# Optimization experiments

Measured on AMD Instinct MI355X. Metric: run time of the kernel, lower is better.

Reference implementation:

```python
import jax, jax.numpy as jnp
import numpy as np

EMBED_DIM = 2048
NUM_HEADS = 16
HEAD_DIM = EMBED_DIM // NUM_HEADS
B, T = 4, 2048


def setup_inputs() -> dict:
    key = jax.random.key(0)
    ks = jax.random.split(key, 9)
    s = 1.0 / np.sqrt(EMBED_DIM)
    x = jax.random.normal(ks[0], (B, T, EMBED_DIM), dtype=jnp.float32)
    Wq = jax.random.normal(ks[1], (EMBED_DIM, EMBED_DIM), dtype=jnp.float32) * s
    bq = jnp.zeros((EMBED_DIM,), dtype=jnp.float32)
    Wk = jax.random.normal(ks[2], (EMBED_DIM, EMBED_DIM), dtype=jnp.float32) * s
    bk = jnp.zeros((EMBED_DIM,), dtype=jnp.float32)
    Wv = jax.random.normal(ks[3], (EMBED_DIM, EMBED_DIM), dtype=jnp.float32) * s
    bv = jnp.zeros((EMBED_DIM,), dtype=jnp.float32)
    Wo = jax.random.normal(ks[4], (EMBED_DIM, EMBED_DIM), dtype=jnp.float32) * s
    bo = jnp.zeros((EMBED_DIM,), dtype=jnp.float32)
    return {"x": x, "Wq": Wq, "bq": bq, "Wk": Wk, "bk": bk,
            "Wv": Wv, "bv": bv, "Wo": Wo, "bo": bo}


def reference(x, Wq, bq, Wk, bk, Wv, bv, Wo, bo):
    Bb, Tt, C = x.shape
    H, D = NUM_HEADS, C // NUM_HEADS
    # QKV projections (Linear: x @ W.T + b), reshape to [B, H, T, D]
    q = (jnp.einsum('btc,oc->bto', x, Wq) + bq).reshape(Bb, Tt, H, D).transpose(0, 2, 1, 3)
    k = (jnp.einsum('btc,oc->bto', x, Wk) + bk).reshape(Bb, Tt, H, D).transpose(0, 2, 1, 3)
    v = (jnp.einsum('btc,oc->bto', x, Wv) + bv).reshape(Bb, Tt, H, D).transpose(0, 2, 1, 3)
    logits = jnp.einsum('bhqd,bhkd->bhqk', q, k) / jnp.sqrt(jnp.float32(D))
    causal = jnp.triu(jnp.ones((Tt, Tt), dtype=bool), 1)  # True above diagonal
    logits = jnp.where(causal, -jnp.inf, logits)
    attn = jax.nn.softmax(logits, axis=-1)
    out = jnp.einsum('bhqk,bhkd->bhqd', attn, v)  # [B, H, T, D]
    out = out.transpose(0, 2, 1, 3).reshape(Bb, Tt, C)
    y = jnp.einsum('btc,oc->bto', out, Wo) + bo
    return y
```

## Files before the change

kernel.cpp:

```cpp
#include <hip/hip_runtime.h>
#include <hip/hip_bf16.h>
#include <cstdint>
#include <cstddef>

typedef __attribute__((ext_vector_type(8))) short short8;
typedef __attribute__((ext_vector_type(4))) short short4_;
typedef __attribute__((ext_vector_type(4))) float floatx4;
typedef __attribute__((ext_vector_type(4))) unsigned short ushort4_;

#define MFMA16(a, b, c) __builtin_amdgcn_mfma_f32_16x16x32_bf16((a), (b), (c), 0, 0, 0)

__device__ __forceinline__ unsigned short f2bf(float f) {
  __hip_bfloat16 h = __float2bfloat16(f);
  return *reinterpret_cast<unsigned short*>(&h);
}

__device__ __forceinline__ void gl_lds16(const void* g, void* lds) {
  __builtin_amdgcn_global_load_lds(
      (const __attribute__((address_space(1))) void*)g,
      (__attribute__((address_space(3))) void*)lds, 16, 0, 0);
}

__global__ void cast5_f32_bf16(const float* __restrict__ x, const float* __restrict__ wq,
                               const float* __restrict__ wk, const float* __restrict__ wv,
                               const float* __restrict__ wo,
                               __hip_bfloat16* __restrict__ xb, __hip_bfloat16* __restrict__ wqb,
                               __hip_bfloat16* __restrict__ wkb, __hip_bfloat16* __restrict__ wvb,
                               __hip_bfloat16* __restrict__ wob) {
  const int bid = blockIdx.x;
  const float* src;
  __hip_bfloat16* dst;
  int base;
  if (bid < 16384)      { src = x;  dst = xb;  base = bid; }
  else if (bid < 20480) { src = wq; dst = wqb; base = bid - 16384; }
  else if (bid < 24576) { src = wk; dst = wkb; base = bid - 20480; }
  else if (bid < 28672) { src = wv; dst = wvb; base = bid - 24576; }
  else                  { src = wo; dst = wob; base = bid - 28672; }
  const int i = base * 1024 + threadIdx.x * 4;
  const float4 v = *reinterpret_cast<const float4*>(src + i);
  ushort4_ o = { f2bf(v.x), f2bf(v.y), f2bf(v.z), f2bf(v.w) };
  *reinterpret_cast<ushort4_*>(dst + i) = o;
}

template <int MODE>
__global__ __launch_bounds__(512, 2)
void gemm256p(const __hip_bfloat16* __restrict__ Ap, const __hip_bfloat16* __restrict__ Bp,
              const float* __restrict__ bias, void* __restrict__ Cout,
              int M, int N, int K) {
  __shared__ __align__(16) __hip_bfloat16 SA[4][256 * 32];
  __shared__ __align__(16) __hip_bfloat16 SB[4][256 * 32];

  const int tid = threadIdx.x;
  const int wid = tid >> 6, lane = tid & 63;
  const int wr = wid >> 2, wc = wid & 3;
  const int g = lane >> 4, c16 = lane & 15;

  const int nbn = N >> 8;
  const int cpx = gridDim.x >> 3;
  const int swzb = (blockIdx.x & 7) * cpx + (blockIdx.x >> 3);
  const int bm = swzb / nbn, bn = swzb % nbn;

  const int srow = lane >> 2;
  const int slog = (lane & 3) ^ ((lane >> 3) & 3);
  const int swz = c16 * 32 + (g ^ ((c16 >> 1) & 3)) * 8;

  floatx4 acc[8][4] = {};
  short8 afA[4], afB[4], bf[4];

  auto stage_i = [&](int kt, int i) {
    const int kb = kt * 32;
    const int slot = kt & 3;
    const int rbase = i * 128 + wid * 16;
    gl_lds16(Ap + (size_t)(bm * 256 + rbase + srow) * K + kb + slog * 8,
             SA[slot] + rbase * 32);
    gl_lds16(Bp + (size_t)(bn * 256 + rbase + srow) * K + kb + slog * 8,
             SB[slot] + rbase * 32);
  };

  auto readA = [&](int slot, int half, short8* af) {
    const __hip_bfloat16* sa = SA[slot];
#pragma unroll
    for (int m = 0; m < 4; ++m)
      af[m] = *reinterpret_cast<const short8*>(sa + wr * 4096 + (half * 4 + m) * 512 + swz);
  };
  auto readB = [&](int slot) {
    const __hip_bfloat16* sb = SB[slot];
#pragma unroll
    for (int n = 0; n < 4; ++n)
      bf[n] = *reinterpret_cast<const short8*>(sb + wc * 2048 + n * 512 + swz);
  };
  auto mfma16 = [&](short8* af, int mh) {
    __builtin_amdgcn_s_setprio(1);
#pragma unroll
    for (int m = 0; m < 4; ++m)
#pragma unroll
      for (int n = 0; n < 4; ++n)
        acc[mh * 4 + m][n] = MFMA16(af[m], bf[n], acc[mh * 4 + m][n]);
    __builtin_amdgcn_s_setprio(0);
  };

  const int nkt = K >> 5;
  stage_i(0, 0); stage_i(0, 1);
  stage_i(1, 0); stage_i(1, 1);
  stage_i(2, 0); stage_i(2, 1);
  asm volatile("s_waitcnt vmcnt(8)" ::: "memory");
  __builtin_amdgcn_s_barrier();

  for (int kt = 0; kt < nkt - 3; ++kt) {
    const int s = kt & 3;
    readA(s, 0, afA);
    readB(s);
    stage_i(kt + 3, 0);
    asm volatile("" ::: "memory");
    __builtin_amdgcn_s_barrier();
    mfma16(afA, 0);
    asm volatile("" ::: "memory");
    __builtin_amdgcn_s_barrier();
    readA(s, 1, afB);
    stage_i(kt + 3, 1);
    asm volatile("s_waitcnt vmcnt(8)" ::: "memory");
    __builtin_amdgcn_s_barrier();
    mfma16(afB, 1);
    asm volatile("" ::: "memory");
    __builtin_amdgcn_s_barrier();
  }
#pragma unroll
  for (int t = 0; t < 3; ++t) {
    const int kt = nkt - 3 + t;
    const int s = kt & 3;
    readA(s, 0, afA);
    readB(s);
    asm volatile("" ::: "memory");
    __builtin_amdgcn_s_barrier();
    mfma16(afA, 0);
    asm volatile("" ::: "memory");
    __builtin_amdgcn_s_barrier();
    readA(s, 1, afB);
    if (t == 0) asm volatile("s_waitcnt vmcnt(4)" ::: "memory");
    else if (t == 1) asm volatile("s_waitcnt vmcnt(0)" ::: "memory");
    __builtin_amdgcn_s_barrier();
    mfma16(afB, 1);
    asm volatile("" ::: "memory");
    __builtin_amdgcn_s_barrier();
  }

#pragma unroll
  for (int n = 0; n < 4; ++n) {
    const int colg = bn * 256 + wc * 64 + n * 16 + c16;
    const float bv = bias[colg];
#pragma unroll
    for (int m = 0; m < 8; ++m) {
      const int rowg = bm * 256 + wr * 128 + m * 16 + g * 4;
      if (MODE == 0) {
        __hip_bfloat16* C = (__hip_bfloat16*)Cout;
#pragma unroll
        for (int j = 0; j < 4; ++j)
          C[(size_t)(rowg + j) * N + colg] = __float2bfloat16(acc[m][n][j] + bv);
      } else if (MODE == 1) {
        __hip_bfloat16* C = (__hip_bfloat16*)Cout;
        const int bb = rowg >> 11, t0 = rowg & 2047;
        ushort4_ pk = { f2bf(acc[m][n][0] + bv), f2bf(acc[m][n][1] + bv),
                        f2bf(acc[m][n][2] + bv), f2bf(acc[m][n][3] + bv) };
        *reinterpret_cast<ushort4_*>(C + ((size_t)bb * 2048 + colg) * 2048 + t0) = pk;
      } else {
        float* C = (float*)Cout;
#pragma unroll
        for (int j = 0; j < 4; ++j)
          C[(size_t)(rowg + j) * N + colg] = acc[m][n][j] + bv;
      }
    }
  }
}

__global__ __launch_bounds__(256, 2)
void attn_fwd7(const __hip_bfloat16* __restrict__ Q, const __hip_bfloat16* __restrict__ K,
               const __hip_bfloat16* __restrict__ Vt, __hip_bfloat16* __restrict__ ctx) {
  constexpr int T = 2048, C = 2048, D = 128;
  __shared__ __align__(16) __hip_bfloat16 Ks[64 * 128];
  __shared__ __align__(16) __hip_bfloat16 Vs[128 * 64];
  __shared__ __align__(16) __hip_bfloat16 Pl[4][16 * 64];

  const int tid = threadIdx.x;
  const int w = tid >> 6, lane = tid & 63;
  const int g = lane >> 4, c16 = lane & 15;

  const int bid = blockIdx.x;
  const int x = bid & 7;
  const int i = bid >> 3;
  const int lo = i & 3, hi = i >> 5;
  const int bh = x * 8 + ((i >> 2) & 7);
  const int qb = (int)((0xF12C4A97865B3DE0ull >> (4 * (hi * 4 + lo))) & 15);
  const int b = bh >> 4, h = bh & 15;
  const int wq = qb * 128 + w * 32;

  const __hip_bfloat16* Qh = Q + (size_t)b * T * C + h * D;
  const __hip_bfloat16* Kh = K + (size_t)b * T * C + h * D;
  const __hip_bfloat16* Vh = Vt + (size_t)bh * D * T;

  short8 qf[2][4];
#pragma unroll
  for (int m = 0; m < 2; ++m)
#pragma unroll
    for (int kk = 0; kk < 4; ++kk)
      qf[m][kk] = *reinterpret_cast<const short8*>(Qh + (size_t)(wq + m * 16 + c16) * C + kk * 32 + g * 8);

  floatx4 acc[2][8] = {};
  float mrow[2] = {-INFINITY, -INFINITY};
  float lrow[2] = {0.f, 0.f};

  const float scale = 0.08838834764831845f;
  const int krow = tid >> 4;
  const int kslot = (tid & 15) ^ (krow & 7);
  const int kgcol = (tid & 15) * 8;
  const int vrow = tid >> 3;
  const int vslot = (tid & 7) ^ (vrow & 7);
  const int vgcol = (tid & 7) * 8;

  short8 kr[4], vr[4];
  auto gloadK = [&](int kb) {
#pragma unroll
    for (int p = 0; p < 4; ++p)
      kr[p] = *reinterpret_cast<const short8*>(Kh + (size_t)(kb + p * 16 + krow) * C + kgcol);
  };
  auto gloadV = [&](int kb) {
#pragma unroll
    for (int p = 0; p < 4; ++p)
      vr[p] = *reinterpret_cast<const short8*>(Vh + (size_t)(p * 32 + vrow) * T + kb + vgcol);
  };

  __hip_bfloat16* Pq = Pl[w];
  const int nkt = qb * 2 + 2;
  gloadK(0);
  gloadV(0);

  for (int kt = 0; kt < nkt; ++kt) {
    const int kb = kt * 64;
    __syncthreads();
#pragma unroll
    for (int p = 0; p < 4; ++p)
      *reinterpret_cast<short8*>(&Ks[(p * 16 + krow) * 128 + kslot * 8]) = kr[p];
#pragma unroll
    for (int p = 0; p < 4; ++p)
      *reinterpret_cast<short8*>(&Vs[(p * 32 + vrow) * 64 + vslot * 8]) = vr[p];
    __syncthreads();

    const bool hasnext = (kt + 1 < nkt);
    const bool part = (kb <= wq + 31);
    if (hasnext) gloadK(kb + 64);

    short8 pb[2][2];
    if (part) {
      const bool needmask = (kb + 63 > wq);
      floatx4 s[2][4] = {};
      __builtin_amdgcn_s_setprio(1);
#pragma unroll
      for (int n = 0; n < 4; ++n)
#pragma unroll
        for (int kk = 0; kk < 4; ++kk) {
          short8 kf = *reinterpret_cast<const short8*>(
              &Ks[(n * 16 + c16) * 128 + (((kk * 4 + g) ^ (c16 & 7)) * 8)]);
          s[0][n] = MFMA16(kf, qf[0][kk], s[0][n]);
          s[1][n] = MFMA16(kf, qf[1][kk], s[1][n]);
        }
      __builtin_amdgcn_s_setprio(0);
      float vmax[2];
#pragma unroll
      for (int m = 0; m < 2; ++m) {
        const int q = wq + m * 16 + c16;
        float vm = -INFINITY;
#pragma unroll
        for (int n = 0; n < 4; ++n)
#pragma unroll
          for (int j = 0; j < 4; ++j) {
            float a = s[m][n][j] * scale;
            if (needmask && (kb + n * 16 + g * 4 + j > q)) a = -INFINITY;
            s[m][n][j] = a;
            vm = fmaxf(vm, a);
          }
        vm = fmaxf(vm, __shfl_xor(vm, 16));
        vm = fmaxf(vm, __shfl_xor(vm, 32));
        vmax[m] = vm;
      }
      const float grow = fmaxf(vmax[0] - mrow[0], vmax[1] - mrow[1]);
      const bool nore = __all(grow <= 8.0f);
#pragma unroll
      for (int m = 0; m < 2; ++m) {
        const float mn = nore ? mrow[m] : fmaxf(mrow[m], vmax[m]);
        float rs = 0.f;
#pragma unroll
        for (int n = 0; n < 4; ++n) {
          float p0 = __expf(s[m][n][0] - mn), p1 = __expf(s[m][n][1] - mn);
          float p2 = __expf(s[m][n][2] - mn), p3 = __expf(s[m][n][3] - mn);
          rs += (p0 + p1) + (p2 + p3);
          ushort4_ pk = { f2bf(p0), f2bf(p1), f2bf(p2), f2bf(p3) };
          *reinterpret_cast<ushort4_*>(&Pq[c16 * 64 + (((4 * n + g) ^ c16) * 4)]) = pk;
        }
        rs += __shfl_xor(rs, 16);
        rs += __shfl_xor(rs, 32);
        if (nore) {
          lrow[m] += rs;
        } else {
          const float sc = __expf(mrow[m] - mn);
          lrow[m] = lrow[m] * sc + rs;
          mrow[m] = mn;
#pragma unroll
          for (int dt = 0; dt < 8; ++dt)
#pragma unroll
            for (int j = 0; j < 4; ++j) acc[m][dt][j] *= sc;
        }
#pragma unroll
        for (int ks = 0; ks < 2; ++ks) {
          short4_ lo2 = *reinterpret_cast<const short4_*>(&Pq[c16 * 64 + (((8 * ks + 2 * g) ^ c16) * 4)]);
          short4_ hi2 = *reinterpret_cast<const short4_*>(&Pq[c16 * 64 + (((8 * ks + 2 * g + 1) ^ c16) * 4)]);
          short8 r;
          r[0] = lo2[0]; r[1] = lo2[1]; r[2] = lo2[2]; r[3] = lo2[3];
          r[4] = hi2[0]; r[5] = hi2[1]; r[6] = hi2[2]; r[7] = hi2[3];
          pb[m][ks] = r;
        }
      }
    }
    if (hasnext) gloadV(kb + 64);
    if (part) {
      __builtin_amdgcn_s_setprio(1);
#pragma unroll
      for (int dt = 0; dt < 8; ++dt)
#pragma unroll
        for (int ks = 0; ks < 2; ++ks) {
          const int pslot = ((ks * 4 + g) ^ (c16 & 7)) * 8;
          short8 vf = *reinterpret_cast<const short8*>(&Vs[(dt * 16 + c16) * 64 + pslot]);
          acc[0][dt] = MFMA16(vf, pb[0][ks], acc[0][dt]);
          acc[1][dt] = MFMA16(vf, pb[1][ks], acc[1][dt]);
        }
      __builtin_amdgcn_s_setprio(0);
    }
  }

#pragma unroll
  for (int m = 0; m < 2; ++m) {
    const float inv = 1.0f / lrow[m];
    const size_t row = (size_t)b * T + wq + m * 16 + c16;
#pragma unroll
    for (int dt = 0; dt < 8; ++dt) {
      ushort4_ o = { f2bf(acc[m][dt][0] * inv), f2bf(acc[m][dt][1] * inv),
                     f2bf(acc[m][dt][2] * inv), f2bf(acc[m][dt][3] * inv) };
      *reinterpret_cast<ushort4_*>(ctx + row * C + h * D + dt * 16 + g * 4) = o;
    }
  }
}

extern "C" void kernel_launch(void* const* d_in, const int* in_sizes, int n_in,
                              void* d_out, int out_size, void* d_ws, size_t ws_size,
                              hipStream_t stream) {
  const float* x  = (const float*)d_in[0];
  const float* Wq = (const float*)d_in[1];
  const float* bq = (const float*)d_in[2];
  const float* Wk = (const float*)d_in[3];
  const float* bk = (const float*)d_in[4];
  const float* Wv = (const float*)d_in[5];
  const float* bv = (const float*)d_in[6];
  const float* Wo = (const float*)d_in[7];
  const float* bo = (const float*)d_in[8];

  const int M = 8192, N = 2048, K = 2048;
  const size_t MB = 1u << 20;
  char* ws = (char*)d_ws;
  __hip_bfloat16* xb  = (__hip_bfloat16*)(ws);
  __hip_bfloat16* wqb = (__hip_bfloat16*)(ws + 32 * MB);
  __hip_bfloat16* wkb = (__hip_bfloat16*)(ws + 40 * MB);
  __hip_bfloat16* wvb = (__hip_bfloat16*)(ws + 48 * MB);
  __hip_bfloat16* wob = (__hip_bfloat16*)(ws + 56 * MB);
  __hip_bfloat16* Qb  = (__hip_bfloat16*)(ws + 64 * MB);
  __hip_bfloat16* Kb  = (__hip_bfloat16*)(ws + 96 * MB);
  __hip_bfloat16* Vtb = (__hip_bfloat16*)(ws + 128 * MB);
  if (ws_size < 160 * MB) return;

  cast5_f32_bf16<<<32768, 256, 0, stream>>>(x, Wq, Wk, Wv, Wo, xb, wqb, wkb, wvb, wob);

  const dim3 gg((M / 256) * (N / 256));
  gemm256p<0><<<gg, 512, 0, stream>>>(xb, wqb, bq, Qb, M, N, K);
  gemm256p<0><<<gg, 512, 0, stream>>>(xb, wkb, bk, Kb, M, N, K);
  gemm256p<1><<<gg, 512, 0, stream>>>(xb, wvb, bv, Vtb, M, N, K);

  attn_fwd7<<<64 * 16, 256, 0, stream>>>(Qb, Kb, Vtb, xb);

  gemm256p<2><<<gg, 512, 0, stream>>>(xb, wob, bo, d_out, M, N, K);
}
```

Measured before the change: 465.0 us.

## Split attention query tile across 8 waves with 16 rows each

The attention kernel moves from 4 waves of 32 query rows each to 8 waves of 16 rows each per 128-row block, with 512 threads and launch bounds allowing 4 blocks. Per-wave accumulator and score registers are halved, which is meant to raise occupancy and spread the K/V staging loads over more threads. The block-to-query-tile mapping also changes from a hardcoded permutation to pairing tile t with tile 15-t for causal load balance. In exchange, each K/V fragment read from LDS now feeds one MFMA instead of two, lowering LDS reuse.

```diff
diff --git a/kernel.cpp b/kernel.cpp
--- a/kernel.cpp
+++ b/kernel.cpp
@@ -172,13 +172,13 @@
   }
 }
 
-__global__ __launch_bounds__(256, 2)
-void attn_fwd7(const __hip_bfloat16* __restrict__ Q, const __hip_bfloat16* __restrict__ K,
+__global__ __launch_bounds__(512, 4)
+void attn_fwd9(const __hip_bfloat16* __restrict__ Q, const __hip_bfloat16* __restrict__ K,
                const __hip_bfloat16* __restrict__ Vt, __hip_bfloat16* __restrict__ ctx) {
   constexpr int T = 2048, C = 2048, D = 128;
   __shared__ __align__(16) __hip_bfloat16 Ks[64 * 128];
   __shared__ __align__(16) __hip_bfloat16 Vs[128 * 64];
-  __shared__ __align__(16) __hip_bfloat16 Pl[4][16 * 64];
+  __shared__ __align__(16) __hip_bfloat16 Pl[8][16 * 64];
 
   const int tid = threadIdx.x;
   const int w = tid >> 6, lane = tid & 63;
@@ -187,45 +187,42 @@
   const int bid = blockIdx.x;
   const int x = bid & 7;
   const int i = bid >> 3;
-  const int lo = i & 3, hi = i >> 5;
-  const int bh = x * 8 + ((i >> 2) & 7);
-  const int qb = (int)((0xF12C4A97865B3DE0ull >> (4 * (hi * 4 + lo))) & 15);
+  const int bh = x * 8 + ((i >> 1) & 7);
+  const int t = i >> 4;
+  const int qb = (i & 1) ? t : 15 - t;
   const int b = bh >> 4, h = bh & 15;
-  const int wq = qb * 128 + w * 32;
+  const int wq = qb * 128 + w * 16;
 
   const __hip_bfloat16* Qh = Q + (size_t)b * T * C + h * D;
   const __hip_bfloat16* Kh = K + (size_t)b * T * C + h * D;
   const __hip_bfloat16* Vh = Vt + (size_t)bh * D * T;
 
-  short8 qf[2][4];
-#pragma unroll
-  for (int m = 0; m < 2; ++m)
-#pragma unroll
-    for (int kk = 0; kk < 4; ++kk)
-      qf[m][kk] = *reinterpret_cast<const short8*>(Qh + (size_t)(wq + m * 16 + c16) * C + kk * 32 + g * 8);
-
-  floatx4 acc[2][8] = {};
-  float mrow[2] = {-INFINITY, -INFINITY};
-  float lrow[2] = {0.f, 0.f};
+  short8 qf[4];
+#pragma unroll
+  for (int kk = 0; kk < 4; ++kk)
+    qf[kk] = *reinterpret_cast<const short8*>(Qh + (size_t)(wq + c16) * C + kk * 32 + g * 8);
+
+  floatx4 acc[8] = {};
+  float mrow = -INFINITY, lrow = 0.f;
 
   const float scale = 0.08838834764831845f;
-  const int krow = tid >> 4;
-  const int kslot = (tid & 15) ^ (krow & 7);
-  const int kgcol = (tid & 15) * 8;
-  const int vrow = tid >> 3;
-  const int vslot = (tid & 7) ^ (vrow & 7);
-  const int vgcol = (tid & 7) * 8;
-
-  short8 kr[4], vr[4];
+  const int kR = tid >> 4;
+  const int kS = (tid & 15) ^ (kR & 7);
+  const int kC = (tid & 15) * 8;
+  const int vR = tid >> 3;
+  const int vS = (tid & 7) ^ (vR & 7);
+  const int vC = (tid & 7) * 8;
+
+  short8 kr[2], vr[2];
   auto gloadK = [&](int kb) {
 #pragma unroll
-    for (int p = 0; p < 4; ++p)
-      kr[p] = *reinterpret_cast<const short8*>(Kh + (size_t)(kb + p * 16 + krow) * C + kgcol);
+    for (int p = 0; p < 2; ++p)
+      kr[p] = *reinterpret_cast<const short8*>(Kh + (size_t)(kb + p * 32 + kR) * C + kC);
   };
   auto gloadV = [&](int kb) {
 #pragma unroll
-    for (int p = 0; p < 4; ++p)
-      vr[p] = *reinterpret_cast<const short8*>(Vh + (size_t)(p * 32 + vrow) * T + kb + vgcol);
+    for (int p = 0; p < 2; ++p)
+      vr[p] = *reinterpret_cast<const short8*>(Vh + (size_t)(p * 64 + vR) * T + kb + vC);
   };
 
   __hip_bfloat16* Pq = Pl[w];
@@ -237,21 +234,21 @@
     const int kb = kt * 64;
     __syncthreads();
 #pragma unroll
-    for (int p = 0; p < 4; ++p)
-      *reinterpret_cast<short8*>(&Ks[(p * 16 + krow) * 128 + kslot * 8]) = kr[p];
-#pragma unroll
-    for (int p = 0; p < 4; ++p)
-      *reinterpret_cast<short8*>(&Vs[(p * 32 + vrow) * 64 + vslot * 8]) = vr[p];
+    for (int p = 0; p < 2; ++p)
+      *reinterpret_cast<short8*>(&Ks[(p * 32 + kR) * 128 + kS * 8]) = kr[p];
+#pragma unroll
+    for (int p = 0; p < 2; ++p)
+      *reinterpret_cast<short8*>(&Vs[(p * 64 + vR) * 64 + vS * 8]) = vr[p];
     __syncthreads();
 
     const bool hasnext = (kt + 1 < nkt);
-    const bool part = (kb <= wq + 31);
+    const bool part = (kb <= wq + 15);
     if (hasnext) gloadK(kb + 64);
 
-    short8 pb[2][2];
+    short8 pb[2];
     if (part) {
       const bool needmask = (kb + 63 > wq);
-      floatx4 s[2][4] = {};
+      floatx4 s[4] = {};
       __builtin_amdgcn_s_setprio(1);
 #pragma unroll
       for (int n = 0; n < 4; ++n)
@@ -259,64 +256,54 @@
         for (int kk = 0; kk < 4; ++kk) {
           short8 kf = *reinterpret_cast<const short8*>(
               &Ks[(n * 16 + c16) * 128 + (((kk * 4 + g) ^ (c16 & 7)) * 8)]);
-          s[0][n] = MFMA16(kf, qf[0][kk], s[0][n]);
-          s[1][n] = MFMA16(kf, qf[1][kk], s[1][n]);
+          s[n] = MFMA16(kf, qf[kk], s[n]);
         }
       __builtin_amdgcn_s_setprio(0);
-      float vmax[2];
-#pragma unroll
-      for (int m = 0; m < 2; ++m) {
-        const int q = wq + m * 16 + c16;
-        float vm = -INFINITY;
-#pragma unroll
-        for (int n = 0; n < 4; ++n)
-#pragma unroll
-          for (int j = 0; j < 4; ++j) {
-            float a = s[m][n][j] * scale;
-            if (needmask && (kb + n * 16 + g * 4 + j > q)) a = -INFINITY;
-            s[m][n][j] = a;
-            vm = fmaxf(vm, a);
-          }
-        vm = fmaxf(vm, __shfl_xor(vm, 16));
-        vm = fmaxf(vm, __shfl_xor(vm, 32));
-        vmax[m] = vm;
+      const int q = wq + c16;
+      float vm = -INFINITY;
+#pragma unroll
+      for (int n = 0; n < 4; ++n)
+#pragma unroll
+        for (int j = 0; j < 4; ++j) {
+          float a = s[n][j] * scale;
+          if (needmask && (kb + n * 16 + g * 4 + j > q)) a = -INFINITY;
+          s[n][j] = a;
+          vm = fmaxf(vm, a);
+        }
+      vm = fmaxf(vm, __shfl_xor(vm, 16));
+      vm = fmaxf(vm, __shfl_xor(vm, 32));
+      const bool nore = __all(vm - mrow <= 8.0f);
+      const float mn = nore ? mrow : fmaxf(mrow, vm);
+      float rs = 0.f;
+#pragma unroll
+      for (int n = 0; n < 4; ++n) {
+        float p0 = __expf(s[n][0] - mn), p1 = __expf(s[n][1] - mn);
+        float p2 = __expf(s[n][2] - mn), p3 = __expf(s[n][3] - mn);
+        rs += (p0 + p1) + (p2 + p3);
+        ushort4_ pk = { f2bf(p0), f2bf(p1), f2bf(p2), f2bf(p3) };
+        *reinterpret_cast<ushort4_*>(&Pq[c16 * 64 + (((4 * n + g) ^ c16) * 4)]) = pk;
       }
-      const float grow = fmaxf(vmax[0] - mrow[0], vmax[1] - mrow[1]);
-      const bool nore = __all(grow <= 8.0f);
-#pragma unroll
-      for (int m = 0; m < 2; ++m) {
-        const float mn = nore ? mrow[m] : fmaxf(mrow[m], vmax[m]);
-        float rs = 0.f;
-#pragma unroll
-        for (int n = 0; n < 4; ++n) {
-          float p0 = __expf(s[m][n][0] - mn), p1 = __expf(s[m][n][1] - mn);
-          float p2 = __expf(s[m][n][2] - mn), p3 = __expf(s[m][n][3] - mn);
-          rs += (p0 + p1) + (p2 + p3);
-          ushort4_ pk = { f2bf(p0), f2bf(p1), f2bf(p2), f2bf(p3) };
-          *reinterpret_cast<ushort4_*>(&Pq[c16 * 64 + (((4 * n + g) ^ c16) * 4)]) = pk;
-        }
-        rs += __shfl_xor(rs, 16);
-        rs += __shfl_xor(rs, 32);
-        if (nore) {
-          lrow[m] += rs;
-        } else {
-          const float sc = __expf(mrow[m] - mn);
-          lrow[m] = lrow[m] * sc + rs;
-          mrow[m] = mn;
-#pragma unroll
-          for (int dt = 0; dt < 8; ++dt)
-#pragma unroll
-            for (int j = 0; j < 4; ++j) acc[m][dt][j] *= sc;
-        }
-#pragma unroll
-        for (int ks = 0; ks < 2; ++ks) {
-          short4_ lo2 = *reinterpret_cast<const short4_*>(&Pq[c16 * 64 + (((8 * ks + 2 * g) ^ c16) * 4)]);
-          short4_ hi2 = *reinterpret_cast<const short4_*>(&Pq[c16 * 64 + (((8 * ks + 2 * g + 1) ^ c16) * 4)]);
-          short8 r;
-          r[0] = lo2[0]; r[1] = lo2[1]; r[2] = lo2[2]; r[3] = lo2[3];
-          r[4] = hi2[0]; r[5] = hi2[1]; r[6] = hi2[2]; r[7] = hi2[3];
-          pb[m][ks] = r;
-        }
+      rs += __shfl_xor(rs, 16);
+      rs += __shfl_xor(rs, 32);
+      if (nore) {
+        lrow += rs;
+      } else {
+        const float sc = __expf(mrow - mn);
+        lrow = lrow * sc + rs;
+        mrow = mn;
+#pragma unroll
+        for (int dt = 0; dt < 8; ++dt)
+#pragma unroll
+          for (int j = 0; j < 4; ++j) acc[dt][j] *= sc;
+      }
+#pragma unroll
+      for (int ks = 0; ks < 2; ++ks) {
+        short4_ lo2 = *reinterpret_cast<const short4_*>(&Pq[c16 * 64 + (((8 * ks + 2 * g) ^ c16) * 4)]);
+        short4_ hi2 = *reinterpret_cast<const short4_*>(&Pq[c16 * 64 + (((8 * ks + 2 * g + 1) ^ c16) * 4)]);
+        short8 r;
+        r[0] = lo2[0]; r[1] = lo2[1]; r[2] = lo2[2]; r[3] = lo2[3];
+        r[4] = hi2[0]; r[5] = hi2[1]; r[6] = hi2[2]; r[7] = hi2[3];
+        pb[ks] = r;
       }
     }
     if (hasnext) gloadV(kb + 64);
@@ -328,23 +315,19 @@
         for (int ks = 0; ks < 2; ++ks) {
           const int pslot = ((ks * 4 + g) ^ (c16 & 7)) * 8;
           short8 vf = *reinterpret_cast<const short8*>(&Vs[(dt * 16 + c16) * 64 + pslot]);
-          acc[0][dt] = MFMA16(vf, pb[0][ks], acc[0][dt]);
-          acc[1][dt] = MFMA16(vf, pb[1][ks], acc[1][dt]);
+          acc[dt] = MFMA16(vf, pb[ks], acc[dt]);
         }
       __builtin_amdgcn_s_setprio(0);
     }
   }
 
-#pragma unroll
-  for (int m = 0; m < 2; ++m) {
-    const float inv = 1.0f / lrow[m];
-    const size_t row = (size_t)b * T + wq + m * 16 + c16;
-#pragma unroll
-    for (int dt = 0; dt < 8; ++dt) {
-      ushort4_ o = { f2bf(acc[m][dt][0] * inv), f2bf(acc[m][dt][1] * inv),
-                     f2bf(acc[m][dt][2] * inv), f2bf(acc[m][dt][3] * inv) };
-      *reinterpret_cast<ushort4_*>(ctx + row * C + h * D + dt * 16 + g * 4) = o;
-    }
+  const float inv = 1.0f / lrow;
+  const size_t row = (size_t)b * T + wq + c16;
+#pragma unroll
+  for (int dt = 0; dt < 8; ++dt) {
+    ushort4_ o = { f2bf(acc[dt][0] * inv), f2bf(acc[dt][1] * inv),
+                   f2bf(acc[dt][2] * inv), f2bf(acc[dt][3] * inv) };
+    *reinterpret_cast<ushort4_*>(ctx + row * C + h * D + dt * 16 + g * 4) = o;
   }
 }
 
@@ -381,7 +364,7 @@
   gemm256p<0><<<gg, 512, 0, stream>>>(xb, wkb, bk, Kb, M, N, K);
   gemm256p<1><<<gg, 512, 0, stream>>>(xb, wvb, bv, Vtb, M, N, K);
 
-  attn_fwd7<<<64 * 16, 256, 0, stream>>>(Qb, Kb, Vtb, xb);
+  attn_fwd9<<<64 * 16, 512, 0, stream>>>(Qb, Kb, Vtb, xb);
 
   gemm256p<2><<<gg, 512, 0, stream>>>(xb, wob, bo, d_out, M, N, K);
 }
```

Result: no change. 473.3 us (+1.8%).

## Load V fragments directly from global memory instead of staging through LDS

Applied to the files above, without the earlier changes.

The attention kernel stops staging V tiles through shared memory. Each wave now reads its V MFMA operands straight from global (L2-cached) memory, double-buffering one dt step ahead. This frees LDS and removes the V LDS writes and reads, in exchange for redundant global reads of V across the four waves of a block and more exposed global-load latency inside the PV loop. The P scratch layout is also widened to 32 rows per wave.

```diff
diff --git a/kernel.cpp b/kernel.cpp
--- a/kernel.cpp
+++ b/kernel.cpp
@@ -173,12 +173,11 @@
 }
 
 __global__ __launch_bounds__(256, 2)
-void attn_fwd7(const __hip_bfloat16* __restrict__ Q, const __hip_bfloat16* __restrict__ K,
-               const __hip_bfloat16* __restrict__ Vt, __hip_bfloat16* __restrict__ ctx) {
+void attn_fwd10(const __hip_bfloat16* __restrict__ Q, const __hip_bfloat16* __restrict__ K,
+                const __hip_bfloat16* __restrict__ Vt, __hip_bfloat16* __restrict__ ctx) {
   constexpr int T = 2048, C = 2048, D = 128;
   __shared__ __align__(16) __hip_bfloat16 Ks[64 * 128];
-  __shared__ __align__(16) __hip_bfloat16 Vs[128 * 64];
-  __shared__ __align__(16) __hip_bfloat16 Pl[4][16 * 64];
+  __shared__ __align__(16) __hip_bfloat16 Pl[4][32][64];
 
   const int tid = threadIdx.x;
   const int w = tid >> 6, lane = tid & 63;
@@ -212,26 +211,17 @@
   const int krow = tid >> 4;
   const int kslot = (tid & 15) ^ (krow & 7);
   const int kgcol = (tid & 15) * 8;
-  const int vrow = tid >> 3;
-  const int vslot = (tid & 7) ^ (vrow & 7);
-  const int vgcol = (tid & 7) * 8;
-
-  short8 kr[4], vr[4];
+
+  short8 kr[4];
   auto gloadK = [&](int kb) {
 #pragma unroll
     for (int p = 0; p < 4; ++p)
       kr[p] = *reinterpret_cast<const short8*>(Kh + (size_t)(kb + p * 16 + krow) * C + kgcol);
   };
-  auto gloadV = [&](int kb) {
-#pragma unroll
-    for (int p = 0; p < 4; ++p)
-      vr[p] = *reinterpret_cast<const short8*>(Vh + (size_t)(p * 32 + vrow) * T + kb + vgcol);
-  };
-
-  __hip_bfloat16* Pq = Pl[w];
+
+  __hip_bfloat16 (*Pq)[64] = Pl[w];
   const int nkt = qb * 2 + 2;
   gloadK(0);
-  gloadV(0);
 
   for (int kt = 0; kt < nkt; ++kt) {
     const int kb = kt * 64;
@@ -239,18 +229,13 @@
 #pragma unroll
     for (int p = 0; p < 4; ++p)
       *reinterpret_cast<short8*>(&Ks[(p * 16 + krow) * 128 + kslot * 8]) = kr[p];
-#pragma unroll
-    for (int p = 0; p < 4; ++p)
-      *reinterpret_cast<short8*>(&Vs[(p * 32 + vrow) * 64 + vslot * 8]) = vr[p];
     __syncthreads();
 
     const bool hasnext = (kt + 1 < nkt);
     const bool part = (kb <= wq + 31);
     if (hasnext) gloadK(kb + 64);
 
-    short8 pb[2][2];
     if (part) {
-      const bool needmask = (kb + 63 > wq);
       floatx4 s[2][4] = {};
       __builtin_amdgcn_s_setprio(1);
 #pragma unroll
@@ -263,6 +248,7 @@
           s[1][n] = MFMA16(kf, qf[1][kk], s[1][n]);
         }
       __builtin_amdgcn_s_setprio(0);
+      const bool needmask = (kb + 63 > wq);
       float vmax[2];
 #pragma unroll
       for (int m = 0; m < 2; ++m) {
@@ -283,6 +269,7 @@
       }
       const float grow = fmaxf(vmax[0] - mrow[0], vmax[1] - mrow[1]);
       const bool nore = __all(grow <= 8.0f);
+      short8 pb[2][2];
 #pragma unroll
       for (int m = 0; m < 2; ++m) {
         const float mn = nore ? mrow[m] : fmaxf(mrow[m], vmax[m]);
@@ -293,7 +280,7 @@
           float p2 = __expf(s[m][n][2] - mn), p3 = __expf(s[m][n][3] - mn);
           rs += (p0 + p1) + (p2 + p3);
           ushort4_ pk = { f2bf(p0), f2bf(p1), f2bf(p2), f2bf(p3) };
-          *reinterpret_cast<ushort4_*>(&Pq[c16 * 64 + (((4 * n + g) ^ c16) * 4)]) = pk;
+          *reinterpret_cast<ushort4_*>(&Pq[m * 16 + c16][((4 * n + g) ^ c16) * 4]) = pk;
         }
         rs += __shfl_xor(rs, 16);
         rs += __shfl_xor(rs, 32);
@@ -310,27 +297,35 @@
         }
 #pragma unroll
         for (int ks = 0; ks < 2; ++ks) {
-          short4_ lo2 = *reinterpret_cast<const short4_*>(&Pq[c16 * 64 + (((8 * ks + 2 * g) ^ c16) * 4)]);
-          short4_ hi2 = *reinterpret_cast<const short4_*>(&Pq[c16 * 64 + (((8 * ks + 2 * g + 1) ^ c16) * 4)]);
+          short4_ lo2 = *reinterpret_cast<const short4_*>(&Pq[m * 16 + c16][((8 * ks + 2 * g) ^ c16) * 4]);
+          short4_ hi2 = *reinterpret_cast<const short4_*>(&Pq[m * 16 + c16][((8 * ks + 2 * g + 1) ^ c16) * 4]);
           short8 r;
           r[0] = lo2[0]; r[1] = lo2[1]; r[2] = lo2[2]; r[3] = lo2[3];
           r[4] = hi2[0]; r[5] = hi2[1]; r[6] = hi2[2]; r[7] = hi2[3];
           pb[m][ks] = r;
         }
       }
-    }
-    if (hasnext) gloadV(kb + 64);
-    if (part) {
+      short8 vf0[2], vf1[2];
+#pragma unroll
+      for (int ks = 0; ks < 2; ++ks)
+        vf0[ks] = *reinterpret_cast<const short8*>(Vh + (size_t)(c16)*T + kb + ks * 32 + g * 8);
       __builtin_amdgcn_s_setprio(1);
 #pragma unroll
-      for (int dt = 0; dt < 8; ++dt)
+      for (int dt = 0; dt < 8; ++dt) {
+        short8* cur = (dt & 1) ? vf1 : vf0;
+        short8* nx  = (dt & 1) ? vf0 : vf1;
+        if (dt < 7) {
+#pragma unroll
+          for (int ks = 0; ks < 2; ++ks)
+            nx[ks] = *reinterpret_cast<const short8*>(
+                Vh + (size_t)((dt + 1) * 16 + c16) * T + kb + ks * 32 + g * 8);
+        }
 #pragma unroll
         for (int ks = 0; ks < 2; ++ks) {
-          const int pslot = ((ks * 4 + g) ^ (c16 & 7)) * 8;
-          short8 vf = *reinterpret_cast<const short8*>(&Vs[(dt * 16 + c16) * 64 + pslot]);
-          acc[0][dt] = MFMA16(vf, pb[0][ks], acc[0][dt]);
-          acc[1][dt] = MFMA16(vf, pb[1][ks], acc[1][dt]);
-        }
+          acc[0][dt] = MFMA16(cur[ks], pb[0][ks], acc[0][dt]);
+          acc[1][dt] = MFMA16(cur[ks], pb[1][ks], acc[1][dt]);
+        }
+      }
       __builtin_amdgcn_s_setprio(0);
     }
   }
@@ -381,7 +376,7 @@
   gemm256p<0><<<gg, 512, 0, stream>>>(xb, wkb, bk, Kb, M, N, K);
   gemm256p<1><<<gg, 512, 0, stream>>>(xb, wvb, bv, Vtb, M, N, K);
 
-  attn_fwd7<<<64 * 16, 256, 0, stream>>>(Qb, Kb, Vtb, xb);
+  attn_fwd10<<<64 * 16, 256, 0, stream>>>(Qb, Kb, Vtb, xb);
 
   gemm256p<2><<<gg, 512, 0, stream>>>(xb, wob, bo, d_out, M, N, K);
 }
```

After: 579.8 us. 24.7% more time.
